# Optimization experiments

Hardware: AMD Instinct MI355X
Metric: run time of the kernel (lower is better)

The kernel has to match this reference:

```python
import jax, jax.numpy as jnp
import numpy as np

B, T, D, C = 16, 4096, 1024, 128


def setup_inputs() -> dict:
    key = jax.random.key(0)
    ks = jax.random.split(key, 15)

    def w(k, out_dim, in_dim):
        return jax.random.normal(k, (out_dim, in_dim), jnp.float32) / np.sqrt(in_dim).astype(np.float32)

    return {
        "x": jax.random.normal(ks[0], (B, T, D), jnp.float32),
        "Wq": w(ks[1], C, D), "bq": jnp.zeros((C,), jnp.float32),
        "Wk": w(ks[2], C, D), "bk": jnp.zeros((C,), jnp.float32),
        "Wv": w(ks[3], C, D), "bv": jnp.zeros((C,), jnp.float32),
        "Wa": w(ks[4], 1, D), "ba": jnp.zeros((1,), jnp.float32),
        "Wb": w(ks[5], 1, D), "bb": jnp.zeros((1,), jnp.float32),
        "Wg": w(ks[6], C, D), "bg": jnp.zeros((C,), jnp.float32),
        "Wo": w(ks[7], D, C), "bo": jnp.zeros((D,), jnp.float32),
    }


def reference(x, Wq, bq, Wk, bk, Wv, bv, Wa, ba, Wb, bb, Wg, bg, Wo, bo):
    # Projections (torch Linear: y = x @ W.T + b)
    q = x @ Wq.T + bq                                   # (B,T,C)
    k = x @ Wk.T + bk
    k = k / jnp.maximum(jnp.linalg.norm(k, axis=-1, keepdims=True), 1e-12)  # F.normalize
    v = x @ Wv.T + bv
    alpha = jax.nn.sigmoid(x @ Wa.T + ba)               # (B,T,1)
    beta = jax.nn.sigmoid(x @ Wb.T + bb)                # (B,T,1)
    gate = jax.nn.sigmoid(x @ Wg.T + bg)                # (B,T,C)

    Bb, Tt, Dd = x.shape
    Cc = q.shape[-1]

    def step(S, inp):
        q_t, k_t, v_t, a_t, b_t = inp                   # (B,C),(B,C),(B,C),(B,1),(B,1)
        a = a_t[:, :, None]                              # (B,1,1)
        b = b_t[:, :, None]                              # (B,1,1)
        # S @ (a*(I - b*k k^T)) = a*(S - b*(S k) k^T)
        Sk = jnp.einsum('bij,bj->bi', S, k_t)            # (B,C)
        S = a * (S - b * (Sk[:, :, None] * k_t[:, None, :])) \
            + b * (v_t[:, :, None] * k_t[:, None, :])
        o = jnp.einsum('bi,bij->bj', q_t, S)             # (B,C)
        return S, o

    xs = (q.swapaxes(0, 1), k.swapaxes(0, 1), v.swapaxes(0, 1),
          alpha.swapaxes(0, 1), beta.swapaxes(0, 1))     # time-major
    S0 = jnp.zeros((Bb, Cc, Cc), x.dtype)
    _, o = jax.lax.scan(step, S0, xs)                    # o: (T,B,C)
    o = o.swapaxes(0, 1) * gate                          # (B,T,C)
    return o @ Wo.T + bo                                 # (B,T,D)
```

## Files before the change

kernel.cpp:

```cpp
#include <hip/hip_runtime.h>
#include <hip/hip_bf16.h>
#include <math.h>

#define NB 16
#define NT 4096
#define ND 1024
#define NCC 128
#define LCH 64
#define NCHUNK 64
#define BTROWS 65536

typedef __bf16 v8bf __attribute__((ext_vector_type(8)));
typedef float  v4f  __attribute__((ext_vector_type(4)));

static __device__ __forceinline__ float sig_(float x){ return 1.0f/(1.0f + __expf(-x)); }
static __device__ __forceinline__ float dot4_(float4 a, float4 b){
    return a.x*b.x + a.y*b.y + a.z*b.z + a.w*b.w;
}

static __device__ __forceinline__ v8bf pack8(float4 a, float4 b){
    v8bf v;
    v[0]=(__bf16)a.x; v[1]=(__bf16)a.y; v[2]=(__bf16)a.z; v[3]=(__bf16)a.w;
    v[4]=(__bf16)b.x; v[5]=(__bf16)b.y; v[6]=(__bf16)b.z; v[7]=(__bf16)b.w;
    return v;
}

static __device__ __forceinline__ void gload16(const void* g, void* l){
    __builtin_amdgcn_global_load_lds(
        (const __attribute__((address_space(1))) unsigned int*)g,
        (__attribute__((address_space(3))) unsigned int*)l, 16, 0, 0);
}

__global__ __launch_bounds__(256) void k_xcast(
    const float* __restrict__ x, const float* __restrict__ Wa,
    const float* __restrict__ Wb, const float* __restrict__ ba,
    const float* __restrict__ bb2, __bf16* __restrict__ xbf,
    float* __restrict__ ab, float* __restrict__ beb)
{
    const int tid = threadIdx.x;
    const int w = tid >> 6, lane = tid & 63;
    const size_t row = (size_t)blockIdx.x*4 + w;
    const float* xr = x + row*ND + lane*16;
    float4 f0 = ((const float4*)xr)[0];
    float4 f1 = ((const float4*)xr)[1];
    float4 f2 = ((const float4*)xr)[2];
    float4 f3 = ((const float4*)xr)[3];
    const float4* wa = (const float4*)(Wa + lane*16);
    const float4* wb = (const float4*)(Wb + lane*16);
    float da = dot4_(f0,wa[0]) + dot4_(f1,wa[1]) + dot4_(f2,wa[2]) + dot4_(f3,wa[3]);
    float db = dot4_(f0,wb[0]) + dot4_(f1,wb[1]) + dot4_(f2,wb[2]) + dot4_(f3,wb[3]);
    __bf16* xd = xbf + row*ND + lane*16;
    *(v8bf*)(xd)   = pack8(f0,f1);
    *(v8bf*)(xd+8) = pack8(f2,f3);
    #pragma unroll
    for (int m=1;m<64;m<<=1){ da += __shfl_xor(da,m,64); db += __shfl_xor(db,m,64); }
    if (lane == 0){
        ab[row]  = sig_(da + ba[0]);
        beb[row] = sig_(db + bb2[0]);
    }
}

__global__ __launch_bounds__(256) void k_wcast(
    const float* __restrict__ Wq, const float* __restrict__ Wk,
    const float* __restrict__ Wv, const float* __restrict__ Wg,
    __bf16* __restrict__ wbf)
{
    const int tid = threadIdx.x;
    const int w = tid >> 6, lane = tid & 63;
    const int row = blockIdx.x*4 + w;
    const float* src = (row < 128) ? Wq + (size_t)row*ND
                     : (row < 256) ? Wk + (size_t)(row-128)*ND
                     : (row < 384) ? Wv + (size_t)(row-256)*ND
                     :               Wg + (size_t)(row-384)*ND;
    const float4* s4 = (const float4*)(src + lane*16);
    float4 f0=s4[0], f1=s4[1], f2=s4[2], f3=s4[3];
    __bf16* xd = wbf + (size_t)row*ND + lane*16;
    *(v8bf*)(xd)   = pack8(f0,f1);
    *(v8bf*)(xd+8) = pack8(f2,f3);
}

__global__ __launch_bounds__(256) void k_proj2(
    const __bf16* __restrict__ xbf, const __bf16* __restrict__ wbf,
    const float* __restrict__ bq, const float* __restrict__ bk,
    const float* __restrict__ bv, const float* __restrict__ bg,
    float* __restrict__ qb, float* __restrict__ kb2,
    float* __restrict__ vb, float* __restrict__ gb)
{
    __shared__ __attribute__((aligned(16))) __bf16 As[128*64];
    __shared__ __attribute__((aligned(16))) __bf16 Bs[128*64];
    const int tid = threadIdx.x;
    const int lane = tid & 63, w = tid >> 6;
    const int q4 = lane >> 4, l16 = lane & 15;
    const int wm = w >> 1, wn = w & 1;

    const int f = blockIdx.x;
    const int xcd = f & 7, j = f >> 3;
    const int m0 = ((xcd << 6) + (j >> 2)) * 128;
    const int n0 = (j & 3) * 128;

    v4f acc[4][4] = {};

    for (int k0 = 0; k0 < ND; k0 += 64){
        __syncthreads();
        #pragma unroll
        for (int i=0;i<4;i++){
            const int r  = (w*4+i)*8 + (lane >> 3);
            const int ce = (((lane & 7) ^ (r & 7)) << 3);
            gload16(xbf + (size_t)(m0 + r)*ND + k0 + ce, (char*)As + (w*4+i)*1024);
            gload16(wbf + (size_t)(n0 + r)*ND + k0 + ce, (char*)Bs + (w*4+i)*1024);
        }
        __syncthreads();
        #pragma unroll
        for (int ks=0; ks<2; ks++){
            v8bf af[4], bf[4];
            #pragma unroll
            for (int mf=0; mf<4; mf++){
                const int r = wm*64 + mf*16 + l16;
                af[mf] = *(const v8bf*)((const char*)As + r*128 + (((ks*4+q4) ^ (r&7)) << 4));
            }
            #pragma unroll
            for (int nf=0; nf<4; nf++){
                const int r = wn*64 + nf*16 + l16;
                bf[nf] = *(const v8bf*)((const char*)Bs + r*128 + (((ks*4+q4) ^ (r&7)) << 4));
            }
            #pragma unroll
            for (int mf=0; mf<4; mf++)
                #pragma unroll
                for (int nf=0; nf<4; nf++)
                    acc[mf][nf] = __builtin_amdgcn_mfma_f32_16x16x32_bf16(af[mf], bf[nf], acc[mf][nf], 0,0,0);
        }
    }

    #pragma unroll
    for (int mf=0; mf<4; mf++){
        #pragma unroll
        for (int nf=0; nf<4; nf++){
            const int ng  = n0 + wn*64 + nf*16 + l16;
            const int col = ng & 127;
            const int sel = ng >> 7;
            const float bias = (sel==0) ? bq[col] : (sel==1) ? bk[col]
                             : (sel==2) ? bv[col] : bg[col];
            #pragma unroll
            for (int r2=0;r2<4;r2++){
                const int m = m0 + wm*64 + mf*16 + q4*4 + r2;
                const float val = acc[mf][nf][r2] + bias;
                const size_t off = (size_t)m*NCC + col;
                if      (sel == 0) qb[off]  = val;
                else if (sel == 1) kb2[off] = val;
                else if (sel == 2) vb[off]  = val;
                else               gb[off]  = sig_(val);
            }
        }
    }
}

__global__ __launch_bounds__(256) void k_knorm(float* __restrict__ kb){
    const int tid = threadIdx.x;
    const int w = tid >> 6, lane = tid & 63;
    const size_t row = (size_t)blockIdx.x*4 + w;
    float* kr = kb + row*NCC;
    float a = kr[lane], b = kr[lane+64];
    float ss = a*a + b*b;
    #pragma unroll
    for (int m=1;m<64;m<<=1) ss += __shfl_xor(ss, m, 64);
    float inv = 1.0f / fmaxf(sqrtf(ss), 1e-12f);
    kr[lane] = a*inv; kr[lane+64] = b*inv;
}

#define KSWZ(t, j)   ((t)*132 + ((((((j)>>2) ^ ((t)&7))) << 2) | ((j)&3)))
#define KSWZ4(t, j4) ((t)*132 + ((((j4) ^ ((t)&7))) << 2))
#define TSWZ(row, g) ((row)*72 + ((((g) ^ ((row)&7))) << 3))

#define SOLVE_LOOP(RHS_EXPR) \
    _Pragma("unroll") \
    for (int t=0;t<64;t++){ \
        const float* Gr = &Gsh[t*68]; \
        float s0=0.f,s1=0.f,s2=0.f,s3=0.f; \
        _Pragma("unroll") \
        for (int s4=0; s4+4<=t; s4+=4){ \
            float4 g = *(const float4*)(Gr+s4); \
            s0 += g.x*u[s4]; s1 += g.y*u[s4+1]; s2 += g.z*u[s4+2]; s3 += g.w*u[s4+3]; \
        } \
        _Pragma("unroll") \
        for (int s=(t & ~3); s<t; s++) s0 += Gr[s]*u[s]; \
        u[t] = bsh[t]*((RHS_EXPR) - ((s0+s1)+(s2+s3))); \
    }

__global__ __launch_bounds__(256) void k_phaseA(
    const float* __restrict__ kb, float* __restrict__ vb, __bf16* __restrict__ Mb,
    const float* __restrict__ ab, const float* __restrict__ beb,
    float* __restrict__ lgb, __bf16* __restrict__ PTb, float* __restrict__ Rb)
{
    __shared__ __attribute__((aligned(16))) float Ksh[LCH*132];
    __shared__ __attribute__((aligned(16))) float Vsh[LCH*132];
    __shared__ __attribute__((aligned(16))) float Gsh[LCH*68];
    __shared__ __attribute__((aligned(16))) __bf16 KT [NCC*72];
    __shared__ __attribute__((aligned(16))) __bf16 EUT[NCC*72];
    __shared__ __attribute__((aligned(16))) __bf16 EMT[NCC*72];
    __shared__ float lgs[LCH], bsh[LCH], esh[LCH], gam[LCH];

    const int tid = threadIdx.x;
    const int b = blockIdx.x >> 6;
    const int c = blockIdx.x & 63;
    const size_t base = (size_t)b*NT + (size_t)c*LCH;

    if (tid < LCH){
        float la = __logf(fmaxf(ab[base+tid], 1e-30f));
        float ps = la;
        #pragma unroll
        for (int off=1; off<64; off<<=1){
            float o = __shfl_up(ps, off, 64);
            if ((tid & 63) >= off) ps += o;
        }
        lgs[tid] = ps;
        bsh[tid] = beb[base+tid];
    }
    {
        const int row = tid >> 2, seg = tid & 3;
        const float* ks = kb + (base+row)*NCC + seg*32;
        const float* vs = vb + (base+row)*NCC + seg*32;
        #pragma unroll
        for (int i=0;i<32;i+=4){
            float4 kv = *(const float4*)(ks+i);
            float4 vv = *(const float4*)(vs+i);
            *(float4*)(&Ksh[KSWZ4(row, ((seg*32+i)>>2))]) = kv;
            *(float4*)(&Vsh[row*132 + seg*32 + i]) = vv;
        }
    }
    __syncthreads();
    if (tid < LCH){
        lgb[base+tid] = lgs[tid];
        esh[tid] = __expf(lgs[LCH-1] - lgs[tid]);
        gam[tid] = __expf(lgs[tid]);
    }
    for (int idx = tid; idx < (LCH*(LCH+1))/2; idx += 256){
        int t = (int)((sqrtf(8.f*(float)idx + 1.f) - 1.f)*0.5f);
        while ((t+1)*(t+2)/2 <= idx) t++;
        while (t*(t+1)/2 > idx) t--;
        const int s = idx - (t*(t+1))/2;
        float dot = 0.f;
        #pragma unroll 8
        for (int j4=0;j4<32;j4++){
            float4 u = *(const float4*)(&Ksh[KSWZ4(s,j4)]);
            float4 v = *(const float4*)(&Ksh[KSWZ4(t,j4)]);
            dot += u.x*v.x + u.y*v.y + u.z*v.z + u.w*v.w;
        }
        Gsh[t*68+s] = __expf(lgs[t]-lgs[s])*dot;
    }
    {
        const int j = tid & 127, th = tid >> 7;
        #pragma unroll
        for (int g=0; g<4; g++){
            const int t0 = th*32 + g*8;
            v8bf pk;
            #pragma unroll
            for (int e=0;e<8;e++) pk[e] = (__bf16)Ksh[KSWZ(t0+e, j)];
            *(v8bf*)(&KT[TSWZ(j, (t0>>3))]) = pk;
        }
    }
    __syncthreads();

    {
        const int half = tid >> 7, cix = tid & 127;
        float u[64];
        if (half == 0){
            SOLVE_LOOP(Vsh[t*132 + cix])
            #pragma unroll
            for (int t=0;t<64;t++) vb[(base+t)*NCC + cix] = u[t];
            #pragma unroll
            for (int g=0; g<8; g++){
                v8bf pk;
                #pragma unroll
                for (int e=0;e<8;e++) pk[e] = (__bf16)(esh[g*8+e]*u[g*8+e]);
                *(v8bf*)(&EUT[TSWZ(cix, g)]) = pk;
            }
        } else {
            SOLVE_LOOP(gam[t]*Ksh[KSWZ(t, cix)])
            #pragma unroll
            for (int t=0;t<64;t++) Mb[(base+t)*NCC + cix] = (__bf16)u[t];
            #pragma unroll
            for (int g=0; g<8; g++){
                v8bf pk;
                #pragma unroll
                for (int e=0;e<8;e++) pk[e] = (__bf16)(esh[g*8+e]*u[g*8+e]);
                *(v8bf*)(&EMT[TSWZ(cix, g)]) = pk;
            }
        }
    }
    __syncthreads();

    {
        const int lane = tid & 63, w = tid >> 6;
        const int q4 = lane >> 4, l16 = lane & 15;
        const int wm = w >> 1, wn = w & 1;
        const float gl = gam[LCH-1];
        const size_t pbase = ((size_t)(b*NCHUNK + c))*NCC*NCC;
        {
            v4f pacc[4][4] = {};
            #pragma unroll
            for (int ks=0; ks<2; ks++){
                v8bf af[4], bf[4];
                #pragma unroll
                for (int mf=0; mf<4; mf++)
                    af[mf] = *(const v8bf*)(&KT[TSWZ(wm*64+mf*16+l16, ks*4+q4)]);
                #pragma unroll
                for (int nf=0; nf<4; nf++)
                    bf[nf] = *(const v8bf*)(&EMT[TSWZ(wn*64+nf*16+l16, ks*4+q4)]);
                #pragma unroll
                for (int mf=0; mf<4; mf++)
                    #pragma unroll
                    for (int nf=0; nf<4; nf++)
                        pacc[mf][nf] = __builtin_amdgcn_mfma_f32_16x16x32_bf16(af[mf], bf[nf], pacc[mf][nf], 0,0,0);
            }
            #pragma unroll
            for (int mf=0; mf<4; mf++){
                #pragma unroll
                for (int nf=0; nf<4; nf++){
                    const int m = wn*64 + nf*16 + l16;
                    #pragma unroll
                    for (int r=0;r<4;r++){
                        const int j = wm*64 + mf*16 + q4*4 + r;
                        float v = -pacc[mf][nf][r];
                        if (j == m) v += gl;
                        PTb[pbase + (size_t)j*NCC + m] = (__bf16)v;
                    }
                }
            }
        }
        {
            v4f racc[4][4] = {};
            #pragma unroll
            for (int ks=0; ks<2; ks++){
                v8bf af[4], bf[4];
                #pragma unroll
                for (int mf=0; mf<4; mf++)
                    af[mf] = *(const v8bf*)(&EUT[TSWZ(wm*64+mf*16+l16, ks*4+q4)]);
                #pragma unroll
                for (int nf=0; nf<4; nf++)
                    bf[nf] = *(const v8bf*)(&KT[TSWZ(wn*64+nf*16+l16, ks*4+q4)]);
                #pragma unroll
                for (int mf=0; mf<4; mf++)
                    #pragma unroll
                    for (int nf=0; nf<4; nf++)
                        racc[mf][nf] = __builtin_amdgcn_mfma_f32_16x16x32_bf16(af[mf], bf[nf], racc[mf][nf], 0,0,0);
            }
            #pragma unroll
            for (int mf=0; mf<4; mf++){
                #pragma unroll
                for (int nf=0; nf<4; nf++){
                    const int jj = wn*64 + nf*16 + l16;
                    #pragma unroll
                    for (int r=0;r<4;r++){
                        const int i = wm*64 + mf*16 + q4*4 + r;
                        Rb[pbase + (size_t)i*NCC + jj] = racc[mf][nf][r];
                    }
                }
            }
        }
    }
}

__global__ __launch_bounds__(256) void k_phaseB(
    const __bf16* __restrict__ PTb, const float* __restrict__ Rb, float* __restrict__ Sb)
{
    __shared__ __attribute__((aligned(16))) float Ssh[16*132];
    const int tid = threadIdx.x;
    const int b = blockIdx.x >> 3, rb = blockIdx.x & 7;
    const int r0 = rb*16;
    const int lane = tid & 63, w = tid >> 6;
    const int q4 = lane >> 4, l16 = lane & 15;
    for (int i=tid; i<16*132; i+=256) Ssh[i] = 0.f;
    __syncthreads();
    for (int c=0; c<NCHUNK; c++){
        const size_t pbase = ((size_t)(b*NCHUNK + c))*NCC*NCC;
        {
            const int row = tid >> 4, cg = (tid & 15)*8;
            float* dst = Sb + pbase + (size_t)(r0+row)*NCC + cg;
            *(float4*)(dst)   = *(const float4*)(&Ssh[row*132+cg]);
            *(float4*)(dst+4) = *(const float4*)(&Ssh[row*132+cg+4]);
        }
        if (c == NCHUNK-1) break;
        v8bf af[4];
        #pragma unroll
        for (int ks=0; ks<4; ks++){
            const float* sr = &Ssh[l16*132 + ks*32 + q4*8];
            v8bf t;
            #pragma unroll
            for (int j=0;j<8;j++) t[j] = (__bf16)sr[j];
            af[ks] = t;
        }
        __syncthreads();
        v4f acc[2] = {};
        #pragma unroll
        for (int nt=0; nt<2; nt++){
            const int n0 = w*32 + nt*16;
            #pragma unroll
            for (int ks=0; ks<4; ks++){
                v8bf bf = *(const v8bf*)(PTb + pbase + (size_t)(n0+l16)*NCC + ks*32 + q4*8);
                acc[nt] = __builtin_amdgcn_mfma_f32_16x16x32_bf16(af[ks], bf, acc[nt], 0,0,0);
            }
        }
        #pragma unroll
        for (int nt=0; nt<2; nt++){
            const int n = w*32 + nt*16 + l16;
            #pragma unroll
            for (int r=0;r<4;r++){
                const int rowl = q4*4 + r;
                Ssh[rowl*132 + n] = acc[nt][r] + Rb[pbase + (size_t)(r0+rowl)*NCC + n];
            }
        }
        __syncthreads();
    }
}

__global__ __launch_bounds__(256) void k_phaseC(
    const float* __restrict__ qb, const float* __restrict__ kb,
    const float* __restrict__ Ub, const __bf16* __restrict__ Mb,
    const float* __restrict__ Sb, const float* __restrict__ lgb,
    float* __restrict__ gb)
{
    __shared__ __attribute__((aligned(16))) __bf16 S0r[NCC*136];
    __shared__ __attribute__((aligned(16))) __bf16 S0t[NCC*136];
    __shared__ __attribute__((aligned(16))) __bf16 MA [LCH*136];
    __shared__ __attribute__((aligned(16))) __bf16 Wsh[LCH*136];
    __shared__ __attribute__((aligned(16))) __bf16 KT [NCC*72];
    __shared__ float lgs[LCH];

    const int tid = threadIdx.x;
    const int b = blockIdx.x >> 6, c = blockIdx.x & 63;
    const size_t base = (size_t)b*NT + (size_t)c*LCH;
    const size_t pbase = ((size_t)(b*NCHUNK + c))*NCC*NCC;
    const int lane = tid & 63, w = tid >> 6;
    const int q4 = lane >> 4, l16 = lane & 15;

    if (tid < LCH) lgs[tid] = lgb[base+tid];
    {
        const int i = tid >> 1, jh = (tid & 1)*64;
        const float* src = Sb + pbase + (size_t)i*NCC + jh;
        #pragma unroll
        for (int g=0; g<8; g++){
            float4 a = *(const float4*)(src + g*8);
            float4 d = *(const float4*)(src + g*8 + 4);
            v8bf pk = pack8(a,d);
            *(v8bf*)(&S0r[i*136 + jh + g*8]) = pk;
            #pragma unroll
            for (int e=0;e<8;e++) S0t[(jh + g*8 + e)*136 + i] = pk[e];
        }
    }
    {
        const int row = tid >> 2, seg = (tid & 3)*32;
        const __bf16* ms = Mb + (base+row)*NCC + seg;
        *(v8bf*)(&MA[row*136 + seg])      = *(const v8bf*)(ms);
        *(v8bf*)(&MA[row*136 + seg + 8])  = *(const v8bf*)(ms+8);
        *(v8bf*)(&MA[row*136 + seg + 16]) = *(const v8bf*)(ms+16);
        *(v8bf*)(&MA[row*136 + seg + 24]) = *(const v8bf*)(ms+24);
    }
    {
        const int j = tid & 127, th = tid >> 7;
        #pragma unroll
        for (int g=0; g<4; g++){
            const int sg = th*4 + g;
            const int s0 = sg*8;
            v8bf pk;
            #pragma unroll
            for (int e=0;e<8;e++) pk[e] = (__bf16)kb[(base+s0+e)*NCC + j];
            *(v8bf*)(&KT[TSWZ(j, sg)]) = pk;
        }
    }
    v8bf qf[4];
    #pragma unroll
    for (int ks=0; ks<4; ks++){
        const float* qs = qb + (base + w*16 + l16)*NCC + ks*32 + q4*8;
        float4 a = *(const float4*)(qs);
        float4 d = *(const float4*)(qs+4);
        qf[ks] = pack8(a,d);
    }
    __syncthreads();

    {
        v4f x1[8] = {};
        #pragma unroll
        for (int ks=0; ks<4; ks++){
            v8bf af = *(const v8bf*)(&MA[(w*16+l16)*136 + ks*32 + q4*8]);
            #pragma unroll
            for (int ib=0; ib<8; ib++){
                v8bf bf = *(const v8bf*)(&S0r[(ib*16+l16)*136 + ks*32 + q4*8]);
                x1[ib] = __builtin_amdgcn_mfma_f32_16x16x32_bf16(af, bf, x1[ib], 0,0,0);
            }
        }
        #pragma unroll
        for (int ib=0; ib<8; ib++){
            #pragma unroll
            for (int r=0;r<4;r++){
                const int t = w*16 + q4*4 + r;
                const int i = ib*16 + l16;
                const float u = Ub[(base+t)*NCC + i];
                Wsh[t*136 + i] = (__bf16)(u - x1[ib][r]);
            }
        }
    }
    v4f o2[8] = {};
    #pragma unroll
    for (int ks=0; ks<4; ks++){
        #pragma unroll
        for (int jb=0; jb<8; jb++){
            v8bf bf = *(const v8bf*)(&S0t[(jb*16+l16)*136 + ks*32 + q4*8]);
            o2[jb] = __builtin_amdgcn_mfma_f32_16x16x32_bf16(qf[ks], bf, o2[jb], 0,0,0);
        }
    }
    __syncthreads();

    {
        v4f x2[4] = {};
        #pragma unroll
        for (int ks=0; ks<4; ks++){
            #pragma unroll
            for (int sb=0; sb<4; sb++){
                v8bf bf = *(const v8bf*)(&Wsh[(sb*16+l16)*136 + ks*32 + q4*8]);
                x2[sb] = __builtin_amdgcn_mfma_f32_16x16x32_bf16(qf[ks], bf, x2[sb], 0,0,0);
            }
        }
        #pragma unroll
        for (int sb=0; sb<4; sb++){
            #pragma unroll
            for (int r=0;r<4;r++){
                const int t = w*16 + q4*4 + r;
                const int s = sb*16 + l16;
                const float v = (s <= t) ? __expf(lgs[t]-lgs[s])*x2[sb][r] : 0.f;
                MA[t*72 + ((((s>>3) ^ (t&7))) << 3) + (s&7)] = (__bf16)v;
            }
        }
    }
    __syncthreads();

    {
        v4f o1[8] = {};
        #pragma unroll
        for (int ks=0; ks<2; ks++){
            v8bf af = *(const v8bf*)(&MA[TSWZ(w*16+l16, ks*4+q4)]);
            #pragma unroll
            for (int jb=0; jb<8; jb++){
                v8bf bf = *(const v8bf*)(&KT[TSWZ(jb*16+l16, ks*4+q4)]);
                o1[jb] = __builtin_amdgcn_mfma_f32_16x16x32_bf16(af, bf, o1[jb], 0,0,0);
            }
        }
        float gam4[4];
        #pragma unroll
        for (int r=0;r<4;r++) gam4[r] = __expf(lgs[w*16 + q4*4 + r]);
        #pragma unroll
        for (int jb=0; jb<8; jb++){
            #pragma unroll
            for (int r=0;r<4;r++){
                const int t = w*16 + q4*4 + r;
                const int j = jb*16 + l16;
                const size_t off = (size_t)(base+t)*NCC + j;
                gb[off] = (o1[jb][r] + gam4[r]*o2[jb][r]) * gb[off];
            }
        }
    }
}

__global__ __launch_bounds__(256) void k_out(
    const float* __restrict__ ob, const float* __restrict__ Wo,
    const float* __restrict__ bo, float* __restrict__ out)
{
    __shared__ __attribute__((aligned(16))) __bf16 As[128*40];
    __shared__ __attribute__((aligned(16))) __bf16 Bs[64*40];
    const int tid = threadIdx.x;
    const int m0 = blockIdx.x*128, n0 = blockIdx.y*64;
    const int lane = tid & 63, w = tid >> 6;
    const int q4 = lane >> 4, l16 = lane & 15;
    const int arow = tid >> 1, aseg = tid & 1;
    const int brow = tid >> 2, bseg = tid & 3;
    const float* asrc = ob + (size_t)(m0+arow)*NCC;
    const float* bsrc = Wo + (size_t)(n0+brow)*NCC;

    v4f acc[2][4] = {};

    for (int k0=0; k0<NCC; k0+=32){
        __syncthreads();
        {
            float4 f0 = *(const float4*)(asrc + k0 + aseg*16);
            float4 f1 = *(const float4*)(asrc + k0 + aseg*16 + 4);
            float4 f2 = *(const float4*)(asrc + k0 + aseg*16 + 8);
            float4 f3 = *(const float4*)(asrc + k0 + aseg*16 + 12);
            *(v8bf*)(&As[arow*40 + aseg*16])     = pack8(f0,f1);
            *(v8bf*)(&As[arow*40 + aseg*16 + 8]) = pack8(f2,f3);
        }
        {
            float4 g0 = *(const float4*)(bsrc + k0 + bseg*8);
            float4 g1 = *(const float4*)(bsrc + k0 + bseg*8 + 4);
            *(v8bf*)(&Bs[brow*40 + bseg*8]) = pack8(g0,g1);
        }
        __syncthreads();
        v8bf af0 = *(const v8bf*)(&As[(w*32 + l16)*40 + q4*8]);
        v8bf af1 = *(const v8bf*)(&As[(w*32 + 16 + l16)*40 + q4*8]);
        #pragma unroll
        for (int nt=0; nt<4; nt++){
            v8bf bf = *(const v8bf*)(&Bs[(nt*16 + l16)*40 + q4*8]);
            acc[0][nt] = __builtin_amdgcn_mfma_f32_16x16x32_bf16(af0, bf, acc[0][nt], 0,0,0);
            acc[1][nt] = __builtin_amdgcn_mfma_f32_16x16x32_bf16(af1, bf, acc[1][nt], 0,0,0);
        }
    }
    #pragma unroll
    for (int mt=0; mt<2; mt++){
        #pragma unroll
        for (int nt=0; nt<4; nt++){
            const int n = n0 + nt*16 + l16;
            const float bias = bo[n];
            #pragma unroll
            for (int r=0;r<4;r++){
                const int m = m0 + w*32 + mt*16 + q4*4 + r;
                out[(size_t)m*ND + n] = acc[mt][nt][r] + bias;
            }
        }
    }
}

extern "C" void kernel_launch(void* const* d_in, const int* in_sizes, int n_in,
                              void* d_out, int out_size, void* d_ws, size_t ws_size,
                              hipStream_t stream)
{
    const float* x  = (const float*)d_in[0];
    const float* Wq = (const float*)d_in[1];
    const float* bq = (const float*)d_in[2];
    const float* Wk = (const float*)d_in[3];
    const float* bk = (const float*)d_in[4];
    const float* Wv = (const float*)d_in[5];
    const float* bv = (const float*)d_in[6];
    const float* Wa = (const float*)d_in[7];
    const float* ba = (const float*)d_in[8];
    const float* Wb = (const float*)d_in[9];
    const float* bb2= (const float*)d_in[10];
    const float* Wg = (const float*)d_in[11];
    const float* bg = (const float*)d_in[12];
    const float* Wo = (const float*)d_in[13];
    const float* bo = (const float*)d_in[14];

    char* ws = (char*)d_ws;
    const size_t SZ = (size_t)BTROWS*NCC*4;
    float*  qb  = (float*)(ws + 0*SZ);
    float*  kb  = (float*)(ws + 1*SZ);
    float*  vb  = (float*)(ws + 2*SZ);
    __bf16* Mb  = (__bf16*)(ws + 3*SZ);
    float*  gb  = (float*)(ws + 4*SZ);
    float*  Sb  = (float*)(ws + 5*SZ);
    float*  Rb  = (float*)(ws + 7*SZ);
    __bf16* PTb = (__bf16*)(ws + 9*SZ);
    float*  ab  = (float*)(ws + 10*SZ);
    float*  beb = (float*)(ws + 10*SZ + 262144);
    float*  lgb = (float*)(ws + 10*SZ + 524288);
    __bf16* xbf = (__bf16*)(ws + 5*SZ);
    __bf16* wbf = (__bf16*)(ws + 9*SZ);
    if (ws_size < 10*SZ + 786432) return;

    dim3 blk(256);
    k_wcast <<<dim3(128),            blk, 0, stream>>>(Wq,Wk,Wv,Wg,wbf);
    k_xcast <<<dim3(BTROWS/4),       blk, 0, stream>>>(x,Wa,Wb,ba,bb2,xbf,ab,beb);
    k_proj2 <<<dim3(2048),           blk, 0, stream>>>(xbf,wbf,bq,bk,bv,bg,qb,kb,vb,gb);
    k_knorm <<<dim3(BTROWS/4),       blk, 0, stream>>>(kb);
    k_phaseA<<<dim3(NB*NCHUNK),      blk, 0, stream>>>(kb, vb, Mb, ab, beb, lgb, PTb, Rb);
    k_phaseB<<<dim3(NB*8),           blk, 0, stream>>>(PTb, Rb, Sb);
    k_phaseC<<<dim3(NB*NCHUNK),      blk, 0, stream>>>(qb, kb, vb, Mb, Sb, lgb, gb);
    k_out   <<<dim3(BTROWS/128, 16), blk, 0, stream>>>(gb, Wo, bo, (float*)d_out);
}
```

Baseline: 1.073 ms.

## Compute chunk Gram matrix with split-bf16 MFMA and shrink phaseA shared memory

In phaseA, K is stored in shared memory as a bf16 hi/lo pair, and the 64x64 Gram matrix K K^T is computed with three bf16 MFMAs per tile instead of scalar fp32 dot products. Shared buffers are aliased into one 66 KB region, which drops the separate V and fp32 K copies and allows two blocks per CU through launch bounds. V is loaded straight into registers, and the triangular solve is unified across both halves. The PT and R stores are vectorized. The split-bf16 trick gives close to fp32 accuracy for G, and the added register pressure from 2-block occupancy could cause spills.

```diff
diff --git a/kernel.cpp b/kernel.cpp
--- a/kernel.cpp
+++ b/kernel.cpp
@@ -11,6 +11,7 @@
 #define BTROWS 65536
 
 typedef __bf16 v8bf __attribute__((ext_vector_type(8)));
+typedef __bf16 v4bf __attribute__((ext_vector_type(4)));
 typedef float  v4f  __attribute__((ext_vector_type(4)));
 
 static __device__ __forceinline__ float sig_(float x){ return 1.0f/(1.0f + __expf(-x)); }
@@ -167,42 +168,41 @@
     kr[lane] = a*inv; kr[lane+64] = b*inv;
 }
 
-#define KSWZ(t, j)   ((t)*132 + ((((((j)>>2) ^ ((t)&7))) << 2) | ((j)&3)))
-#define KSWZ4(t, j4) ((t)*132 + ((((j4) ^ ((t)&7))) << 2))
-#define TSWZ(row, g) ((row)*72 + ((((g) ^ ((row)&7))) << 3))
-
-#define SOLVE_LOOP(RHS_EXPR) \
-    _Pragma("unroll") \
-    for (int t=0;t<64;t++){ \
-        const float* Gr = &Gsh[t*68]; \
-        float s0=0.f,s1=0.f,s2=0.f,s3=0.f; \
-        _Pragma("unroll") \
-        for (int s4=0; s4+4<=t; s4+=4){ \
-            float4 g = *(const float4*)(Gr+s4); \
-            s0 += g.x*u[s4]; s1 += g.y*u[s4+1]; s2 += g.z*u[s4+2]; s3 += g.w*u[s4+3]; \
-        } \
-        _Pragma("unroll") \
-        for (int s=(t & ~3); s<t; s++) s0 += Gr[s]*u[s]; \
-        u[t] = bsh[t]*((RHS_EXPR) - ((s0+s1)+(s2+s3))); \
-    }
-
-__global__ __launch_bounds__(256) void k_phaseA(
+#define TSW(r, g)  ((r)*64 + ((((g) ^ ((r)&7))) << 3))
+
+static __device__ __forceinline__ int kswz(int t, int g){
+    return t*128 + (((g & 8) | ((g & 7) ^ (t & 7))) << 3);
+}
+
+__global__ __launch_bounds__(256, 2) void k_phaseA(
     const float* __restrict__ kb, float* __restrict__ vb, __bf16* __restrict__ Mb,
     const float* __restrict__ ab, const float* __restrict__ beb,
     float* __restrict__ lgb, __bf16* __restrict__ PTb, float* __restrict__ Rb)
 {
-    __shared__ __attribute__((aligned(16))) float Ksh[LCH*132];
-    __shared__ __attribute__((aligned(16))) float Vsh[LCH*132];
-    __shared__ __attribute__((aligned(16))) float Gsh[LCH*68];
-    __shared__ __attribute__((aligned(16))) __bf16 KT [NCC*72];
-    __shared__ __attribute__((aligned(16))) __bf16 EUT[NCC*72];
-    __shared__ __attribute__((aligned(16))) __bf16 EMT[NCC*72];
-    __shared__ float lgs[LCH], bsh[LCH], esh[LCH], gam[LCH];
+    __shared__ __attribute__((aligned(16))) char SM[67584];
+    __bf16* KH  = (__bf16*)(SM);
+    __bf16* KL  = (__bf16*)(SM + 16384);
+    float*  Gsh = (float*) (SM + 32768);
+    __bf16* EMT = (__bf16*)(SM + 50176);
+    float*  lgs = (float*) (SM + 66560);
+    float*  bsh = (float*) (SM + 66816);
+    float*  esh = (float*) (SM + 67072);
+    float*  gam = (float*) (SM + 67328);
+    __bf16* KT  = (__bf16*)(SM + 16384);
+    __bf16* EUT = (__bf16*)(SM + 32768);
 
     const int tid = threadIdx.x;
-    const int b = blockIdx.x >> 6;
-    const int c = blockIdx.x & 63;
+    const int b = blockIdx.x >> 6, c = blockIdx.x & 63;
     const size_t base = (size_t)b*NT + (size_t)c*LCH;
+    const int lane = tid & 63, w = tid >> 6;
+    const int q4 = lane >> 4, l16 = lane & 15;
+    const int half = tid >> 7, cix = tid & 127;
+
+    float u[64];
+    if (half == 0){
+        #pragma unroll
+        for (int t=0;t<64;t++) u[t] = vb[(base+t)*NCC + cix];
+    }
 
     if (tid < LCH){
         float la = __logf(fmaxf(ab[base+tid], 1e-30f));
@@ -217,14 +217,20 @@
     }
     {
         const int row = tid >> 2, seg = tid & 3;
-        const float* ks = kb + (base+row)*NCC + seg*32;
-        const float* vs = vb + (base+row)*NCC + seg*32;
-        #pragma unroll
-        for (int i=0;i<32;i+=4){
-            float4 kv = *(const float4*)(ks+i);
-            float4 vv = *(const float4*)(vs+i);
-            *(float4*)(&Ksh[KSWZ4(row, ((seg*32+i)>>2))]) = kv;
-            *(float4*)(&Vsh[row*132 + seg*32 + i]) = vv;
+        const float* ksr = kb + (base+row)*NCC + seg*32;
+        #pragma unroll
+        for (int gs=0; gs<4; gs++){
+            float4 a = *(const float4*)(ksr + gs*8);
+            float4 d = *(const float4*)(ksr + gs*8 + 4);
+            v8bf hi = pack8(a,d);
+            v8bf lo;
+            lo[0]=(__bf16)(a.x-(float)hi[0]); lo[1]=(__bf16)(a.y-(float)hi[1]);
+            lo[2]=(__bf16)(a.z-(float)hi[2]); lo[3]=(__bf16)(a.w-(float)hi[3]);
+            lo[4]=(__bf16)(d.x-(float)hi[4]); lo[5]=(__bf16)(d.y-(float)hi[5]);
+            lo[6]=(__bf16)(d.z-(float)hi[6]); lo[7]=(__bf16)(d.w-(float)hi[7]);
+            const int off = kswz(row, seg*4+gs);
+            *(v8bf*)(&KH[off]) = hi;
+            *(v8bf*)(&KL[off]) = lo;
         }
     }
     __syncthreads();
@@ -233,128 +239,174 @@
         esh[tid] = __expf(lgs[LCH-1] - lgs[tid]);
         gam[tid] = __expf(lgs[tid]);
     }
-    for (int idx = tid; idx < (LCH*(LCH+1))/2; idx += 256){
-        int t = (int)((sqrtf(8.f*(float)idx + 1.f) - 1.f)*0.5f);
-        while ((t+1)*(t+2)/2 <= idx) t++;
-        while (t*(t+1)/2 > idx) t--;
-        const int s = idx - (t*(t+1))/2;
-        float dot = 0.f;
-        #pragma unroll 8
-        for (int j4=0;j4<32;j4++){
-            float4 u = *(const float4*)(&Ksh[KSWZ4(s,j4)]);
-            float4 v = *(const float4*)(&Ksh[KSWZ4(t,j4)]);
-            dot += u.x*v.x + u.y*v.y + u.z*v.z + u.w*v.w;
-        }
-        Gsh[t*68+s] = __expf(lgs[t]-lgs[s])*dot;
-    }
-    {
-        const int j = tid & 127, th = tid >> 7;
-        #pragma unroll
-        for (int g=0; g<4; g++){
-            const int t0 = th*32 + g*8;
-            v8bf pk;
-            #pragma unroll
-            for (int e=0;e<8;e++) pk[e] = (__bf16)Ksh[KSWZ(t0+e, j)];
-            *(v8bf*)(&KT[TSWZ(j, (t0>>3))]) = pk;
+    if (w != 1){
+        const int wt = w >> 1, ws2 = w & 1;
+        v4f g2[2][2] = {};
+        #pragma unroll
+        for (int ks=0; ks<4; ks++){
+            v8bf ah[2], al[2], bh[2], bl[2];
+            #pragma unroll
+            for (int mf=0; mf<2; mf++){
+                const int r = wt*32 + mf*16 + l16;
+                const int off = kswz(r, ks*4+q4);
+                ah[mf] = *(const v8bf*)(&KH[off]);
+                al[mf] = *(const v8bf*)(&KL[off]);
+            }
+            #pragma unroll
+            for (int nf=0; nf<2; nf++){
+                const int r = ws2*32 + nf*16 + l16;
+                const int off = kswz(r, ks*4+q4);
+                bh[nf] = *(const v8bf*)(&KH[off]);
+                bl[nf] = *(const v8bf*)(&KL[off]);
+            }
+            #pragma unroll
+            for (int mf=0; mf<2; mf++)
+                #pragma unroll
+                for (int nf=0; nf<2; nf++){
+                    g2[mf][nf] = __builtin_amdgcn_mfma_f32_16x16x32_bf16(al[mf], bh[nf], g2[mf][nf], 0,0,0);
+                    g2[mf][nf] = __builtin_amdgcn_mfma_f32_16x16x32_bf16(ah[mf], bl[nf], g2[mf][nf], 0,0,0);
+                    g2[mf][nf] = __builtin_amdgcn_mfma_f32_16x16x32_bf16(ah[mf], bh[nf], g2[mf][nf], 0,0,0);
+                }
+        }
+        #pragma unroll
+        for (int mf=0; mf<2; mf++){
+            #pragma unroll
+            for (int nf=0; nf<2; nf++){
+                #pragma unroll
+                for (int r=0;r<4;r++){
+                    const int t = wt*32 + mf*16 + q4*4 + r;
+                    const int s = ws2*32 + nf*16 + l16;
+                    if (s <= t) Gsh[t*68+s] = __expf(lgs[t]-lgs[s])*g2[mf][nf][r];
+                }
+            }
         }
     }
     __syncthreads();
 
-    {
-        const int half = tid >> 7, cix = tid & 127;
-        float u[64];
+    if (half == 1){
+        const int gc = cix >> 3, ge = cix & 7;
+        #pragma unroll
+        for (int t=0;t<64;t++){
+            const int off = t*128 + (((gc&8) | ((gc&7)^(t&7))) << 3) + ge;
+            u[t] = gam[t]*((float)KH[off] + (float)KL[off]);
+        }
+    }
+    #pragma unroll
+    for (int t=0;t<64;t++){
+        const float* Gr = &Gsh[t*68];
+        float s0=0.f,s1=0.f,s2=0.f,s3=0.f;
+        #pragma unroll
+        for (int s4=0; s4+4<=t; s4+=4){
+            float4 g = *(const float4*)(Gr+s4);
+            s0 += g.x*u[s4]; s1 += g.y*u[s4+1]; s2 += g.z*u[s4+2]; s3 += g.w*u[s4+3];
+        }
+        #pragma unroll
+        for (int s=(t & ~3); s<t; s++) s0 += Gr[s]*u[s];
+        u[t] = bsh[t]*(u[t] - ((s0+s1)+(s2+s3)));
+    }
+    if (half == 0){
+        #pragma unroll
+        for (int t=0;t<64;t++) vb[(base+t)*NCC + cix] = u[t];
+    } else {
+        #pragma unroll
+        for (int t=0;t<64;t++) Mb[(base+t)*NCC + cix] = (__bf16)u[t];
+    }
+    __syncthreads();
+
+    {
         if (half == 0){
-            SOLVE_LOOP(Vsh[t*132 + cix])
-            #pragma unroll
-            for (int t=0;t<64;t++) vb[(base+t)*NCC + cix] = u[t];
             #pragma unroll
             for (int g=0; g<8; g++){
                 v8bf pk;
                 #pragma unroll
                 for (int e=0;e<8;e++) pk[e] = (__bf16)(esh[g*8+e]*u[g*8+e]);
-                *(v8bf*)(&EUT[TSWZ(cix, g)]) = pk;
+                *(v8bf*)(&EUT[TSW(cix, g)]) = pk;
             }
         } else {
-            SOLVE_LOOP(gam[t]*Ksh[KSWZ(t, cix)])
-            #pragma unroll
-            for (int t=0;t<64;t++) Mb[(base+t)*NCC + cix] = (__bf16)u[t];
             #pragma unroll
             for (int g=0; g<8; g++){
                 v8bf pk;
                 #pragma unroll
                 for (int e=0;e<8;e++) pk[e] = (__bf16)(esh[g*8+e]*u[g*8+e]);
-                *(v8bf*)(&EMT[TSWZ(cix, g)]) = pk;
-            }
+                *(v8bf*)(&EMT[TSW(cix, g)]) = pk;
+            }
+        }
+        const int j = cix, gc = j >> 3, ge = j & 7;
+        #pragma unroll
+        for (int g2b=0; g2b<4; g2b++){
+            const int tg = half*4 + g2b, t0 = tg*8;
+            v8bf pk;
+            #pragma unroll
+            for (int e=0;e<8;e++)
+                pk[e] = KH[(t0+e)*128 + (((gc&8) | ((gc&7)^((t0+e)&7))) << 3) + ge];
+            *(v8bf*)(&KT[TSW(j, tg)]) = pk;
         }
     }
     __syncthreads();
 
-    {
-        const int lane = tid & 63, w = tid >> 6;
-        const int q4 = lane >> 4, l16 = lane & 15;
-        const int wm = w >> 1, wn = w & 1;
-        const float gl = gam[LCH-1];
-        const size_t pbase = ((size_t)(b*NCHUNK + c))*NCC*NCC;
-        {
-            v4f pacc[4][4] = {};
-            #pragma unroll
-            for (int ks=0; ks<2; ks++){
-                v8bf af[4], bf[4];
-                #pragma unroll
-                for (int mf=0; mf<4; mf++)
-                    af[mf] = *(const v8bf*)(&KT[TSWZ(wm*64+mf*16+l16, ks*4+q4)]);
+    const int wm = w >> 1, wn = w & 1;
+    const float gl = gam[LCH-1];
+    const size_t pbase = ((size_t)(b*NCHUNK + c))*NCC*NCC;
+    {
+        v4f pacc[4][4] = {};
+        #pragma unroll
+        for (int ks=0; ks<2; ks++){
+            v8bf af[4], bf[4];
+            #pragma unroll
+            for (int mf=0; mf<4; mf++)
+                af[mf] = *(const v8bf*)(&EMT[TSW(wm*64+mf*16+l16, ks*4+q4)]);
+            #pragma unroll
+            for (int nf=0; nf<4; nf++)
+                bf[nf] = *(const v8bf*)(&KT[TSW(wn*64+nf*16+l16, ks*4+q4)]);
+            #pragma unroll
+            for (int mf=0; mf<4; mf++)
                 #pragma unroll
                 for (int nf=0; nf<4; nf++)
-                    bf[nf] = *(const v8bf*)(&EMT[TSWZ(wn*64+nf*16+l16, ks*4+q4)]);
+                    pacc[mf][nf] = __builtin_amdgcn_mfma_f32_16x16x32_bf16(af[mf], bf[nf], pacc[mf][nf], 0,0,0);
+        }
+        #pragma unroll
+        for (int mf=0; mf<4; mf++){
+            #pragma unroll
+            for (int nf=0; nf<4; nf++){
+                const int m0 = wm*64 + mf*16 + q4*4;
+                const int j  = wn*64 + nf*16 + l16;
+                v4bf pk;
                 #pragma unroll
-                for (int mf=0; mf<4; mf++)
-                    #pragma unroll
-                    for (int nf=0; nf<4; nf++)
-                        pacc[mf][nf] = __builtin_amdgcn_mfma_f32_16x16x32_bf16(af[mf], bf[nf], pacc[mf][nf], 0,0,0);
-            }
-            #pragma unroll
-            for (int mf=0; mf<4; mf++){
-                #pragma unroll
-                for (int nf=0; nf<4; nf++){
-                    const int m = wn*64 + nf*16 + l16;
-                    #pragma unroll
-                    for (int r=0;r<4;r++){
-                        const int j = wm*64 + mf*16 + q4*4 + r;
-                        float v = -pacc[mf][nf][r];
-                        if (j == m) v += gl;
-                        PTb[pbase + (size_t)j*NCC + m] = (__bf16)v;
-                    }
+                for (int r=0;r<4;r++){
+                    float v = -pacc[mf][nf][r];
+                    if (j == m0+r) v += gl;
+                    pk[r] = (__bf16)v;
                 }
-            }
-        }
-        {
-            v4f racc[4][4] = {};
-            #pragma unroll
-            for (int ks=0; ks<2; ks++){
-                v8bf af[4], bf[4];
-                #pragma unroll
-                for (int mf=0; mf<4; mf++)
-                    af[mf] = *(const v8bf*)(&EUT[TSWZ(wm*64+mf*16+l16, ks*4+q4)]);
+                *(v4bf*)(PTb + pbase + (size_t)j*NCC + m0) = pk;
+            }
+        }
+    }
+    {
+        v4f racc[4][4] = {};
+        #pragma unroll
+        for (int ks=0; ks<2; ks++){
+            v8bf af[4], bf[4];
+            #pragma unroll
+            for (int mf=0; mf<4; mf++)
+                af[mf] = *(const v8bf*)(&KT[TSW(wm*64+mf*16+l16, ks*4+q4)]);
+            #pragma unroll
+            for (int nf=0; nf<4; nf++)
+                bf[nf] = *(const v8bf*)(&EUT[TSW(wn*64+nf*16+l16, ks*4+q4)]);
+            #pragma unroll
+            for (int mf=0; mf<4; mf++)
                 #pragma unroll
                 for (int nf=0; nf<4; nf++)
-                    bf[nf] = *(const v8bf*)(&KT[TSWZ(wn*64+nf*16+l16, ks*4+q4)]);
-                #pragma unroll
-                for (int mf=0; mf<4; mf++)
-                    #pragma unroll
-                    for (int nf=0; nf<4; nf++)
-                        racc[mf][nf] = __builtin_amdgcn_mfma_f32_16x16x32_bf16(af[mf], bf[nf], racc[mf][nf], 0,0,0);
-            }
-            #pragma unroll
-            for (int mf=0; mf<4; mf++){
-                #pragma unroll
-                for (int nf=0; nf<4; nf++){
-                    const int jj = wn*64 + nf*16 + l16;
-                    #pragma unroll
-                    for (int r=0;r<4;r++){
-                        const int i = wm*64 + mf*16 + q4*4 + r;
-                        Rb[pbase + (size_t)i*NCC + jj] = racc[mf][nf][r];
-                    }
-                }
+                    racc[mf][nf] = __builtin_amdgcn_mfma_f32_16x16x32_bf16(af[mf], bf[nf], racc[mf][nf], 0,0,0);
+        }
+        #pragma unroll
+        for (int mf=0; mf<4; mf++){
+            #pragma unroll
+            for (int nf=0; nf<4; nf++){
+                const int j0 = wm*64 + mf*16 + q4*4;
+                const int i  = wn*64 + nf*16 + l16;
+                float4 fv = make_float4(racc[mf][nf][0], racc[mf][nf][1],
+                                        racc[mf][nf][2], racc[mf][nf][3]);
+                *(float4*)(Rb + pbase + (size_t)i*NCC + j0) = fv;
             }
         }
     }
@@ -464,7 +516,7 @@
             v8bf pk;
             #pragma unroll
             for (int e=0;e<8;e++) pk[e] = (__bf16)kb[(base+s0+e)*NCC + j];
-            *(v8bf*)(&KT[TSWZ(j, sg)]) = pk;
+            *(v8bf*)(&KT[(j)*72 + ((((sg) ^ ((j)&7))) << 3)]) = pk;
         }
     }
     v8bf qf[4];
@@ -537,10 +589,10 @@
         v4f o1[8] = {};
         #pragma unroll
         for (int ks=0; ks<2; ks++){
-            v8bf af = *(const v8bf*)(&MA[TSWZ(w*16+l16, ks*4+q4)]);
+            v8bf af = *(const v8bf*)(&MA[(w*16+l16)*72 + ((((ks*4+q4) ^ ((w*16+l16)&7))) << 3)]);
             #pragma unroll
             for (int jb=0; jb<8; jb++){
-                v8bf bf = *(const v8bf*)(&KT[TSWZ(jb*16+l16, ks*4+q4)]);
+                v8bf bf = *(const v8bf*)(&KT[(jb*16+l16)*72 + ((((ks*4+q4) ^ ((jb*16+l16)&7))) << 3)]);
                 o1[jb] = __builtin_amdgcn_mfma_f32_16x16x32_bf16(af, bf, o1[jb], 0,0,0);
             }
         }
```

New measurement: 968.9 us. 9.7% less time.
